# Optimization experiments

Hardware: AMD Instinct MI355X
Metric: run time of the kernel (lower is better)

Reference implementation:

```python
import jax, jax.numpy as jnp
import numpy as np

B, I, R, A, V = 256, 512, 512, 196, 10000

def _linear_params(key, out_dim, in_dim):
    k1, k2 = jax.random.split(key)
    s = 1.0 / np.sqrt(in_dim)
    W = jax.random.uniform(k1, (out_dim, in_dim), minval=-s, maxval=s, dtype=jnp.float32)
    b = jax.random.uniform(k2, (out_dim,), minval=-s, maxval=s, dtype=jnp.float32)
    return W, b

def setup_inputs() -> dict:
    key = jax.random.key(0)
    ks = jax.random.split(key, 16)
    d = {}
    d['x'] = jax.random.normal(ks[0], (B, I), dtype=jnp.float32)
    d['att'] = jax.random.normal(ks[1], (B, A, R), dtype=jnp.float32)
    d['prev_c'] = jax.random.normal(ks[2], (B, R), dtype=jnp.float32)
    d['prev_h'] = jax.random.normal(ks[3], (B, R), dtype=jnp.float32)
    for i, (name, o, inn) in enumerate([('a2a', A, R), ('h2a', A, R), ('d2d', 1, A),
                                         ('i2h', 4 * R, I), ('a2h', 4 * R, R), ('h2h', 4 * R, R),
                                         ('a2a1', A, R), ('h2a1', A, R), ('d2d1', 1, A),
                                         ('proj', V, R)]):
        W, b = _linear_params(ks[4 + i], o, inn)
        d['W_' + name] = W
        d['b_' + name] = b
    return d

def _lin(x, W, b):
    return x @ W.T + b

def _attend(att, h, Wa, ba, Wh, bh, Wd, bd):
    # att: (B, A, R); h: (B, R)
    av = jnp.einsum('bar,or->bao', att, Wa) + ba        # (B, A, A)
    ah = _lin(h, Wh, bh)                                # (B, A)
    dot = jnp.tanh(av + ah[:, :, None])                 # (B, A, A)
    scores = jnp.einsum('bao,o->ba', dot, Wd[0]) + bd[0]  # (B, A)
    w = jax.nn.softmax(scores, axis=-1)
    return jnp.einsum('bar,ba->br', att, w)             # (B, R)

def reference(x, att, prev_c, prev_h,
              W_a2a, b_a2a, W_h2a, b_h2a, W_d2d, b_d2d,
              W_i2h, b_i2h, W_a2h, b_a2h, W_h2h, b_h2h,
              W_a2a1, b_a2a1, W_h2a1, b_h2a1, W_d2d1, b_d2d1,
              W_proj, b_proj):
    # first attention uses prev_h
    prev_att_res = _attend(att, prev_h, W_a2a, b_a2a, W_h2a, b_h2a, W_d2d, b_d2d)
    sums = _lin(x, W_i2h, b_i2h) + _lin(prev_h, W_h2h, b_h2h) + _lin(prev_att_res, W_a2h, b_a2h)
    sig = jax.nn.sigmoid(sums[:, :3 * R])
    in_gate = sig[:, 0:R]
    forget_gate = sig[:, R:2 * R]
    out_gate = sig[:, 2 * R:3 * R]
    in_transform = jnp.tanh(sums[:, 3 * R:4 * R])
    next_c = forget_gate * prev_c + in_gate * in_transform
    next_h = out_gate * jnp.tanh(next_c)
    # second attention uses next_h
    att_res = _attend(att, next_h, W_a2a1, b_a2a1, W_h2a1, b_h2a1, W_d2d1, b_d2d1)
    top_h = att_res + next_h
    logsoft = jax.nn.log_softmax(_lin(top_h, W_proj, b_proj), axis=-1)
    return next_c, top_h, logsoft
```

## Files before the change

kernel.cpp:

```cpp
#include <hip/hip_runtime.h>
#include <math.h>

constexpr int cB  = 256;
constexpr int cI  = 512;
constexpr int cR  = 512;
constexpr int cA  = 196;
constexpr int cV  = 10000;
constexpr int cH4 = 2048;

typedef short bf16x8 __attribute__((ext_vector_type(8)));
typedef float f32x4  __attribute__((ext_vector_type(4)));
typedef unsigned short us8 __attribute__((ext_vector_type(8)));

__device__ inline unsigned short f2bf(float f) {
    unsigned int u = __float_as_uint(f);
    u += 0x7fffu + ((u >> 16) & 1u);
    return (unsigned short)(u >> 16);
}
__device__ inline float bf2f(unsigned short s) {
    return __uint_as_float(((unsigned int)s) << 16);
}

__global__ __launch_bounds__(256) void k_cvt4(
    const float* __restrict__ s0, unsigned short* __restrict__ d0, int nb0,
    const float* __restrict__ s1, unsigned short* __restrict__ d1, int nb1,
    const float* __restrict__ s2, unsigned short* __restrict__ d2, int nb2,
    const float* __restrict__ s3, unsigned short* __restrict__ d3, int nb3)
{
    int blk = blockIdx.x;
    const float* src; unsigned short* dst; int base;
    if (blk < nb0)                  { src = s0; dst = d0; base = blk; }
    else if (blk < nb0 + nb1)       { src = s1; dst = d1; base = blk - nb0; }
    else if (blk < nb0 + nb1 + nb2) { src = s2; dst = d2; base = blk - nb0 - nb1; }
    else                            { src = s3; dst = d3; base = blk - nb0 - nb1 - nb2; }
    int i = base * 256 + threadIdx.x;
    float4 v = ((const float4*)src)[i];
    ushort4 b;
    b.x = f2bf(v.x); b.y = f2bf(v.y); b.z = f2bf(v.z); b.w = f2bf(v.w);
    ((ushort4*)dst)[i] = b;
}

__global__ __launch_bounds__(256) void k_ah(
    const float* __restrict__ h, const float* __restrict__ W,
    const float* __restrict__ bias, float* __restrict__ out)
{
    __shared__ __align__(16) float h_s[cR];
    int b = blockIdx.x;
    int t = threadIdx.x;
    h_s[t]       = h[b * cR + t];
    h_s[t + 256] = h[b * cR + t + 256];
    __syncthreads();
    if (t < cA) {
        const float4* Wv = (const float4*)(W + (size_t)t * cR);
        const float4* hv = (const float4*)h_s;
        float acc = 0.f;
        #pragma unroll 4
        for (int k = 0; k < cR / 4; ++k) {
            float4 w4 = Wv[k], x4 = hv[k];
            acc += w4.x * x4.x + w4.y * x4.y + w4.z * x4.z + w4.w * x4.w;
        }
        out[b * cA + t] = acc + bias[t];
    }
}

constexpr int SC_LDA = 72;

__global__ __launch_bounds__(256, 3) void k_scores_cv(
    const float* __restrict__ att, unsigned short* __restrict__ att_bf,
    const unsigned short* __restrict__ wa_bf,
    const float* __restrict__ ba, const float* __restrict__ Wd,
    const float* __restrict__ bd, const float* __restrict__ ah,
    float* __restrict__ scores, int wb)
{
    __shared__ __align__(16) unsigned short att_s[64][SC_LDA];
    __shared__ __align__(16) unsigned short wa_s[224][SC_LDA];
    __shared__ float ba_s[224];
    __shared__ float wd_s[224];
    __shared__ float part_s[64][2];

    int tid  = threadIdx.x;
    int wave = tid >> 6;
    int lane = tid & 63;
    int lx   = lane & 15;
    int quad = lane >> 4;
    int mg   = wave >> 1;
    int ng   = wave & 1;
    size_t row0 = (size_t)blockIdx.x * 64;

    if (tid < 224) {
        ba_s[tid] = (tid < cA) ? ba[tid] : 0.f;
        wd_s[tid] = (tid < cA) ? Wd[tid] : 0.f;
    }

    int a_r = tid >> 4, a_c = (tid & 15) * 4;
    int w_r = tid >> 3, w_c = (tid & 7) * 8;
    const float* attA = att + (row0 + a_r) * cR + a_c;
    unsigned short* wbA = att_bf + (row0 + a_r) * cR + a_c;

    f32x4 acc[2][7];
    #pragma unroll
    for (int m = 0; m < 2; ++m)
        #pragma unroll
        for (int c = 0; c < 7; ++c) acc[m][c] = (f32x4){0.f, 0.f, 0.f, 0.f};

    float4 patt[4];
    us8    pwa[7];
    #pragma unroll
    for (int i = 0; i < 4; ++i)
        patt[i] = *(const float4*)(attA + (size_t)i * 16 * cR);
    #pragma unroll
    for (int i = 0; i < 7; ++i) {
        int r = w_r + 32 * i;
        pwa[i] = (r < cA) ? *(const us8*)(wa_bf + (size_t)r * cR + w_c)
                          : (us8){0,0,0,0,0,0,0,0};
    }

    for (int k0 = 0; k0 < cR; k0 += 64) {
        #pragma unroll
        for (int i = 0; i < 4; ++i) {
            float4 v = patt[i];
            ushort4 bv;
            bv.x = f2bf(v.x); bv.y = f2bf(v.y); bv.z = f2bf(v.z); bv.w = f2bf(v.w);
            *(ushort4*)&att_s[a_r + 16 * i][a_c] = bv;
            if (wb)
                *(ushort4*)(wbA + (size_t)i * 16 * cR + k0) = bv;
        }
        #pragma unroll
        for (int i = 0; i < 7; ++i)
            *(us8*)&wa_s[w_r + 32 * i][w_c] = pwa[i];
        if (k0 + 64 < cR) {
            #pragma unroll
            for (int i = 0; i < 4; ++i)
                patt[i] = *(const float4*)(attA + (size_t)i * 16 * cR + k0 + 64);
            #pragma unroll
            for (int i = 0; i < 7; ++i) {
                int r = w_r + 32 * i;
                pwa[i] = (r < cA) ? *(const us8*)(wa_bf + (size_t)r * cR + k0 + 64 + w_c)
                                  : (us8){0,0,0,0,0,0,0,0};
            }
        }
        __syncthreads();
        #pragma unroll
        for (int ks = 0; ks < 2; ++ks) {
            int kb = ks * 32 + quad * 8;
            bf16x8 af[2];
            #pragma unroll
            for (int m = 0; m < 2; ++m)
                af[m] = *(const bf16x8*)&att_s[mg * 32 + m * 16 + lx][kb];
            #pragma unroll
            for (int c = 0; c < 7; ++c) {
                bf16x8 bfr = *(const bf16x8*)&wa_s[ng * 112 + c * 16 + lx][kb];
                #pragma unroll
                for (int m = 0; m < 2; ++m)
                    acc[m][c] = __builtin_amdgcn_mfma_f32_16x16x32_bf16(af[m], bfr, acc[m][c], 0, 0, 0);
            }
        }
        __syncthreads();
    }

    #pragma unroll
    for (int m = 0; m < 2; ++m) {
        #pragma unroll
        for (int reg = 0; reg < 4; ++reg) {
            int rl = mg * 32 + m * 16 + quad * 4 + reg;
            float ahv = ah[row0 + rl];
            float part = 0.f;
            #pragma unroll
            for (int c = 0; c < 7; ++c) {
                int col = ng * 112 + c * 16 + lx;
                part += tanhf(acc[m][c][reg] + ba_s[col] + ahv) * wd_s[col];
            }
            part += __shfl_xor(part, 1);
            part += __shfl_xor(part, 2);
            part += __shfl_xor(part, 4);
            part += __shfl_xor(part, 8);
            if (lx == 0) part_s[rl][ng] = part;
        }
    }
    __syncthreads();
    if (tid < 64)
        scores[row0 + tid] = part_s[tid][0] + part_s[tid][1] + bd[0];
}

__global__ __launch_bounds__(256, 3) void k_scores_bf(
    const unsigned short* __restrict__ att_bf,
    const unsigned short* __restrict__ wa_bf,
    const float* __restrict__ ba, const float* __restrict__ Wd,
    const float* __restrict__ bd, const float* __restrict__ ah,
    float* __restrict__ scores)
{
    __shared__ __align__(16) unsigned short att_s[64][SC_LDA];
    __shared__ __align__(16) unsigned short wa_s[224][SC_LDA];
    __shared__ float ba_s[224];
    __shared__ float wd_s[224];
    __shared__ float part_s[64][2];

    int tid  = threadIdx.x;
    int wave = tid >> 6;
    int lane = tid & 63;
    int lx   = lane & 15;
    int quad = lane >> 4;
    int mg   = wave >> 1;
    int ng   = wave & 1;
    size_t row0 = (size_t)blockIdx.x * 64;

    if (tid < 224) {
        ba_s[tid] = (tid < cA) ? ba[tid] : 0.f;
        wd_s[tid] = (tid < cA) ? Wd[tid] : 0.f;
    }

    int a_r = tid >> 3, a_c = (tid & 7) * 8;
    int w_r = tid >> 3, w_c = (tid & 7) * 8;
    const unsigned short* attA = att_bf + (row0 + a_r) * cR + a_c;

    f32x4 acc[2][7];
    #pragma unroll
    for (int m = 0; m < 2; ++m)
        #pragma unroll
        for (int c = 0; c < 7; ++c) acc[m][c] = (f32x4){0.f, 0.f, 0.f, 0.f};

    us8 patt[2];
    us8 pwa[7];
    #pragma unroll
    for (int i = 0; i < 2; ++i)
        patt[i] = *(const us8*)(attA + (size_t)i * 32 * cR);
    #pragma unroll
    for (int i = 0; i < 7; ++i) {
        int r = w_r + 32 * i;
        pwa[i] = (r < cA) ? *(const us8*)(wa_bf + (size_t)r * cR + w_c)
                          : (us8){0,0,0,0,0,0,0,0};
    }

    for (int k0 = 0; k0 < cR; k0 += 64) {
        #pragma unroll
        for (int i = 0; i < 2; ++i)
            *(us8*)&att_s[a_r + 32 * i][a_c] = patt[i];
        #pragma unroll
        for (int i = 0; i < 7; ++i)
            *(us8*)&wa_s[w_r + 32 * i][w_c] = pwa[i];
        if (k0 + 64 < cR) {
            #pragma unroll
            for (int i = 0; i < 2; ++i)
                patt[i] = *(const us8*)(attA + (size_t)i * 32 * cR + k0 + 64);
            #pragma unroll
            for (int i = 0; i < 7; ++i) {
                int r = w_r + 32 * i;
                pwa[i] = (r < cA) ? *(const us8*)(wa_bf + (size_t)r * cR + k0 + 64 + w_c)
                                  : (us8){0,0,0,0,0,0,0,0};
            }
        }
        __syncthreads();
        #pragma unroll
        for (int ks = 0; ks < 2; ++ks) {
            int kb = ks * 32 + quad * 8;
            bf16x8 af[2];
            #pragma unroll
            for (int m = 0; m < 2; ++m)
                af[m] = *(const bf16x8*)&att_s[mg * 32 + m * 16 + lx][kb];
            #pragma unroll
            for (int c = 0; c < 7; ++c) {
                bf16x8 bfr = *(const bf16x8*)&wa_s[ng * 112 + c * 16 + lx][kb];
                #pragma unroll
                for (int m = 0; m < 2; ++m)
                    acc[m][c] = __builtin_amdgcn_mfma_f32_16x16x32_bf16(af[m], bfr, acc[m][c], 0, 0, 0);
            }
        }
        __syncthreads();
    }

    #pragma unroll
    for (int m = 0; m < 2; ++m) {
        #pragma unroll
        for (int reg = 0; reg < 4; ++reg) {
            int rl = mg * 32 + m * 16 + quad * 4 + reg;
            float ahv = ah[row0 + rl];
            float part = 0.f;
            #pragma unroll
            for (int c = 0; c < 7; ++c) {
                int col = ng * 112 + c * 16 + lx;
                part += tanhf(acc[m][c][reg] + ba_s[col] + ahv) * wd_s[col];
            }
            part += __shfl_xor(part, 1);
            part += __shfl_xor(part, 2);
            part += __shfl_xor(part, 4);
            part += __shfl_xor(part, 8);
            if (lx == 0) part_s[rl][ng] = part;
        }
    }
    __syncthreads();
    if (tid < 64)
        scores[row0 + tid] = part_s[tid][0] + part_s[tid][1] + bd[0];
}

__device__ inline void softmax_w(const float* scores, int b, int t, float* red,
                                 float* w_s)
{
    float s = (t < cA) ? scores[b * cA + t] : -INFINITY;
    red[t] = s; __syncthreads();
    for (int off = 128; off > 0; off >>= 1) {
        if (t < off) red[t] = fmaxf(red[t], red[t + off]);
        __syncthreads();
    }
    float mx = red[0];
    __syncthreads();
    float e = (t < cA) ? expf(s - mx) : 0.f;
    red[t] = e; __syncthreads();
    for (int off = 128; off > 0; off >>= 1) {
        if (t < off) red[t] += red[t + off];
        __syncthreads();
    }
    float inv = 1.f / red[0];
    if (t < cA) w_s[t] = e * inv;
    __syncthreads();
}

__global__ __launch_bounds__(512) void k_attres_bf(
    const float* __restrict__ scores, const unsigned short* __restrict__ att_bf,
    const float* __restrict__ addin,
    float* __restrict__ out, unsigned short* __restrict__ out_bf)
{
    __shared__ float red[512];
    __shared__ float w_s[cA];
    __shared__ float red2[8][512];
    int b = blockIdx.x, t = threadIdx.x;

    float s = (t < cA) ? scores[b * cA + t] : -INFINITY;
    red[t] = s; __syncthreads();
    for (int off = 256; off > 0; off >>= 1) {
        if (t < off) red[t] = fmaxf(red[t], red[t + off]);
        __syncthreads();
    }
    float mx = red[0];
    __syncthreads();
    float e = (t < cA) ? expf(s - mx) : 0.f;
    red[t] = e; __syncthreads();
    for (int off = 256; off > 0; off >>= 1) {
        if (t < off) red[t] += red[t + off];
        __syncthreads();
    }
    float inv = 1.f / red[0];
    if (t < cA) w_s[t] = e * inv;
    __syncthreads();

    int p = t >> 6, l = t & 63;
    const unsigned short* base = att_bf + (size_t)b * cA * cR + l * 8;
    float acc[8] = {};
    #pragma unroll 4
    for (int a = p; a < cA; a += 8) {
        us8 v = *(const us8*)(base + (size_t)a * cR);
        float w = w_s[a];
        #pragma unroll
        for (int j = 0; j < 8; ++j)
            acc[j] += bf2f(v[j]) * w;
    }
    #pragma unroll
    for (int j = 0; j < 8; ++j)
        red2[p][l * 8 + j] = acc[j];
    __syncthreads();
    {
        int r = t;
        float s2 = red2[0][r] + red2[1][r] + red2[2][r] + red2[3][r]
                 + red2[4][r] + red2[5][r] + red2[6][r] + red2[7][r];
        if (addin) s2 += addin[b * cR + r];
        out[b * cR + r] = s2;
        out_bf[b * cR + r] = f2bf(s2);
    }
}

__global__ __launch_bounds__(256) void k_attres_f32(
    const float* __restrict__ scores, const float* __restrict__ att,
    const float* __restrict__ addin,
    float* __restrict__ out, unsigned short* __restrict__ out_bf)
{
    __shared__ float red[256];
    __shared__ float w_s[cA];
    int b = blockIdx.x, t = threadIdx.x;
    softmax_w(scores, b, t, red, w_s);

    const float* attb = att + (size_t)b * cA * cR + 2 * t;
    float acc0 = 0.f, acc1 = 0.f;
    #pragma unroll 4
    for (int a = 0; a < cA; ++a) {
        float2 u = *(const float2*)(attb + (size_t)a * cR);
        float w = w_s[a];
        acc0 += u.x * w;
        acc1 += u.y * w;
    }
    if (addin) {
        acc0 += addin[b * cR + 2 * t];
        acc1 += addin[b * cR + 2 * t + 1];
    }
    out[b * cR + 2 * t]     = acc0;
    out[b * cR + 2 * t + 1] = acc1;
    out_bf[b * cR + 2 * t]     = f2bf(acc0);
    out_bf[b * cR + 2 * t + 1] = f2bf(acc1);
}

__global__ __launch_bounds__(256, 4) void k_sums(
    const unsigned short* __restrict__ x_bf,
    const unsigned short* __restrict__ h_bf,
    const unsigned short* __restrict__ ar_bf,
    const float* __restrict__ Wi, const float* __restrict__ Wh,
    const float* __restrict__ Wa,
    const float* __restrict__ bi, const float* __restrict__ bh,
    const float* __restrict__ ba, float* __restrict__ out)
{
    __shared__ __align__(16) unsigned short a_s[32][SC_LDA];
    __shared__ __align__(16) unsigned short w_s[64][SC_LDA];
    int tid  = threadIdx.x;
    int wave = tid >> 6;
    int lane = tid & 63;
    int lx   = lane & 15;
    int quad = lane >> 4;
    int b0 = blockIdx.x * 32;
    int j0 = blockIdx.y * 64;

    const unsigned short* Aarr[3] = {x_bf, h_bf, ar_bf};
    const float* Warr[3] = {Wi, Wh, Wa};

    int a_r = tid >> 3, a_c = (tid & 7) * 8;
    int w_r = tid >> 4, w_c = (tid & 15) * 4;

    f32x4 acc0 = {0.f, 0.f, 0.f, 0.f}, acc1 = {0.f, 0.f, 0.f, 0.f};

    us8 pa;
    float4 pw[4];
    pa = *(const us8*)(Aarr[0] + (size_t)(b0 + a_r) * cR + a_c);
    #pragma unroll
    for (int i = 0; i < 4; ++i)
        pw[i] = *(const float4*)(Warr[0] + (size_t)(j0 + w_r + 16 * i) * cR + w_c);

    for (int it = 0; it < 24; ++it) {
        *(us8*)&a_s[a_r][a_c] = pa;
        #pragma unroll
        for (int i = 0; i < 4; ++i) {
            float4 v = pw[i];
            ushort4 bv;
            bv.x = f2bf(v.x); bv.y = f2bf(v.y); bv.z = f2bf(v.z); bv.w = f2bf(v.w);
            *(ushort4*)&w_s[w_r + 16 * i][w_c] = bv;
        }
        if (it < 23) {
            int s2 = (it + 1) >> 3, k2 = ((it + 1) & 7) * 64;
            pa = *(const us8*)(Aarr[s2] + (size_t)(b0 + a_r) * cR + k2 + a_c);
            #pragma unroll
            for (int i = 0; i < 4; ++i)
                pw[i] = *(const float4*)(Warr[s2] + (size_t)(j0 + w_r + 16 * i) * cR + k2 + w_c);
        }
        __syncthreads();
        #pragma unroll
// ... 138 lines not shown
    float mx = -INFINITY;
    for (int v = t; v < cV / 4; v += 256) {
        float4 f = row4[v];
        mx = fmaxf(mx, fmaxf(fmaxf(f.x, f.y), fmaxf(f.z, f.w)));
    }
    red[t] = mx; __syncthreads();
    for (int off = 128; off > 0; off >>= 1) {
        if (t < off) red[t] = fmaxf(red[t], red[t + off]);
        __syncthreads();
    }
    mx = red[0]; __syncthreads();
    float sum = 0.f;
    for (int v = t; v < cV / 4; v += 256) {
        float4 f = row4[v];
        sum += expf(f.x - mx) + expf(f.y - mx) + expf(f.z - mx) + expf(f.w - mx);
    }
    red[t] = sum; __syncthreads();
    for (int off = 128; off > 0; off >>= 1) {
        if (t < off) red[t] += red[t + off];
        __syncthreads();
    }
    float lse = mx + logf(red[0]);
    for (int v = t; v < cV / 4; v += 256) {
        float4 f = row4[v];
        f.x -= lse; f.y -= lse; f.z -= lse; f.w -= lse;
        ((float4*)row)[v] = f;
    }
}

extern "C" void kernel_launch(void* const* d_in, const int* in_sizes, int n_in,
                              void* d_out, int out_size, void* d_ws, size_t ws_size,
                              hipStream_t stream)
{
    const float* x      = (const float*)d_in[0];
    const float* att    = (const float*)d_in[1];
    const float* prev_c = (const float*)d_in[2];
    const float* prev_h = (const float*)d_in[3];
    const float* W_a2a  = (const float*)d_in[4];
    const float* b_a2a  = (const float*)d_in[5];
    const float* W_h2a  = (const float*)d_in[6];
    const float* b_h2a  = (const float*)d_in[7];
    const float* W_d2d  = (const float*)d_in[8];
    const float* b_d2d  = (const float*)d_in[9];
    const float* W_i2h  = (const float*)d_in[10];
    const float* b_i2h  = (const float*)d_in[11];
    const float* W_a2h  = (const float*)d_in[12];
    const float* b_a2h  = (const float*)d_in[13];
    const float* W_h2h  = (const float*)d_in[14];
    const float* b_h2h  = (const float*)d_in[15];
    const float* W_a2a1 = (const float*)d_in[16];
    const float* b_a2a1 = (const float*)d_in[17];
    const float* W_h2a1 = (const float*)d_in[18];
    const float* b_h2a1 = (const float*)d_in[19];
    const float* W_d2d1 = (const float*)d_in[20];
    const float* b_d2d1 = (const float*)d_in[21];
    const float* W_proj = (const float*)d_in[22];
    const float* b_proj = (const float*)d_in[23];

    float* out_next_c = (float*)d_out;
    float* out_top_h  = out_next_c + (size_t)cB * cR;
    float* out_logits = out_top_h  + (size_t)cB * cR;

    const size_t ATT_FLOATS = 12845056;
    const size_t NEED_A = (ATT_FLOATS + 1445888) * sizeof(float);
    bool bigws = ws_size >= NEED_A;

    float* ws = (float*)d_ws;
    unsigned short* att_bf = (unsigned short*)ws;
    float* p = bigws ? (ws + ATT_FLOATS) : ws;
    unsigned short* wa2a_bf  = (unsigned short*)p;  p += 50176;
    unsigned short* wa2a1_bf = (unsigned short*)p;  p += 50176;
    unsigned short* x_bf     = (unsigned short*)p;  p += 65536;
    unsigned short* h_bf     = (unsigned short*)p;  p += 65536;
    unsigned short* ar1_bf   = (unsigned short*)p;  p += 65536;
    unsigned short* ar2_bf   = (unsigned short*)p;  p += 65536;
    unsigned short* toph_bf  = (unsigned short*)p;  p += 65536;
    float* ws_ah      = p;  p += 50176;
    float* ws_scores  = p;  p += 50176;
    float* ws_attres1 = p;  p += 131072;
    float* ws_attres2 = p;  p += 131072;
    float* ws_sums    = p;  p += 524288;
    float* ws_next_h  = p;  p += 131072;

    k_cvt4<<<452, 256, 0, stream>>>(W_a2a, wa2a_bf, 98,
                                    W_a2a1, wa2a1_bf, 98,
                                    x, x_bf, 128,
                                    prev_h, h_bf, 128);

    k_ah<<<cB, 256, 0, stream>>>(prev_h, W_h2a, b_h2a, ws_ah);
    k_scores_cv<<<(cB * cA) / 64, 256, 0, stream>>>(att, att_bf, wa2a_bf,
                                                    b_a2a, W_d2d, b_d2d,
                                                    ws_ah, ws_scores,
                                                    bigws ? 1 : 0);
    if (bigws)
        k_attres_bf<<<cB, 512, 0, stream>>>(ws_scores, att_bf, nullptr,
                                            ws_attres1, ar1_bf);
    else
        k_attres_f32<<<cB, 256, 0, stream>>>(ws_scores, att, nullptr,
                                             ws_attres1, ar1_bf);

    k_sums<<<dim3(8, 32), 256, 0, stream>>>(x_bf, h_bf, ar1_bf,
                                            W_i2h, W_h2h, W_a2h,
                                            b_i2h, b_h2h, b_a2h, ws_sums);
    k_cell<<<(cB * cR) / 256, 256, 0, stream>>>(ws_sums, prev_c, out_next_c, ws_next_h);

    k_ah<<<cB, 256, 0, stream>>>(ws_next_h, W_h2a1, b_h2a1, ws_ah);
    if (bigws) {
        k_scores_bf<<<(cB * cA) / 64, 256, 0, stream>>>(att_bf, wa2a1_bf,
                                                        b_a2a1, W_d2d1, b_d2d1,
                                                        ws_ah, ws_scores);
        k_attres_bf<<<cB, 512, 0, stream>>>(ws_scores, att_bf, ws_next_h,
                                            out_top_h, toph_bf);
    } else {
        k_scores_cv<<<(cB * cA) / 64, 256, 0, stream>>>(att, att_bf, wa2a1_bf,
                                                        b_a2a1, W_d2d1, b_d2d1,
                                                        ws_ah, ws_scores, 0);
        k_attres_f32<<<cB, 256, 0, stream>>>(ws_scores, att, ws_next_h,
                                             out_top_h, toph_bf);
    }

    k_lin<<<dim3(2, 157), 256, 0, stream>>>(toph_bf, W_proj, b_proj, out_logits, cV);
    k_logsoftmax<<<cB, 256, 0, stream>>>(out_logits);
}
```

Before: 389.0 us.

## Load whole att row tile into LDS up front in score kernels, halve M tile

The score kernels now process 32 att rows per block instead of 64 and load the full 512-wide row slice of att into shared memory once, before the K loop, instead of streaming 64-column chunks. Only the W_a2a tile is still pipelined per K step, and each wave now does one M fragment. The aim is to issue all att loads early for more memory-level parallelism and more blocks (twice the grid). In exchange the W_a2a tile is reloaded by twice as many blocks, register pressure rises from the 16 prefetched float4s, and occupancy is lowered to 2 blocks per CU.

```diff
diff --git a/kernel.cpp b/kernel.cpp
--- a/kernel.cpp
+++ b/kernel.cpp
@@ -64,19 +64,20 @@
 }
 
 constexpr int SC_LDA = 72;
-
-__global__ __launch_bounds__(256, 3) void k_scores_cv(
+constexpr int AT_LDA = 520;
+
+__global__ __launch_bounds__(256, 2) void k_scores_cv(
     const float* __restrict__ att, unsigned short* __restrict__ att_bf,
     const unsigned short* __restrict__ wa_bf,
     const float* __restrict__ ba, const float* __restrict__ Wd,
     const float* __restrict__ bd, const float* __restrict__ ah,
     float* __restrict__ scores, int wb)
 {
-    __shared__ __align__(16) unsigned short att_s[64][SC_LDA];
+    __shared__ __align__(16) unsigned short att_s[32][AT_LDA];
     __shared__ __align__(16) unsigned short wa_s[224][SC_LDA];
     __shared__ float ba_s[224];
     __shared__ float wd_s[224];
-    __shared__ float part_s[64][2];
+    __shared__ float part_s[32][2];
 
     int tid  = threadIdx.x;
     int wave = tid >> 6;
@@ -85,29 +86,18 @@
     int quad = lane >> 4;
     int mg   = wave >> 1;
     int ng   = wave & 1;
-    size_t row0 = (size_t)blockIdx.x * 64;
-
-    if (tid < 224) {
-        ba_s[tid] = (tid < cA) ? ba[tid] : 0.f;
-        wd_s[tid] = (tid < cA) ? Wd[tid] : 0.f;
-    }
-
-    int a_r = tid >> 4, a_c = (tid & 15) * 4;
+    size_t row0 = (size_t)blockIdx.x * 32;
+
+    const float* attW = att + (row0 + wave * 8) * cR + lane * 4;
+    float4 patt[16];
+    #pragma unroll
+    for (int i = 0; i < 8; ++i) {
+        patt[2 * i]     = *(const float4*)(attW + (size_t)i * cR);
+        patt[2 * i + 1] = *(const float4*)(attW + (size_t)i * cR + 256);
+    }
+
     int w_r = tid >> 3, w_c = (tid & 7) * 8;
-    const float* attA = att + (row0 + a_r) * cR + a_c;
-    unsigned short* wbA = att_bf + (row0 + a_r) * cR + a_c;
-
-    f32x4 acc[2][7];
-    #pragma unroll
-    for (int m = 0; m < 2; ++m)
-        #pragma unroll
-        for (int c = 0; c < 7; ++c) acc[m][c] = (f32x4){0.f, 0.f, 0.f, 0.f};
-
-    float4 patt[4];
-    us8    pwa[7];
-    #pragma unroll
-    for (int i = 0; i < 4; ++i)
-        patt[i] = *(const float4*)(attA + (size_t)i * 16 * cR);
+    us8 pwa[7];
     #pragma unroll
     for (int i = 0; i < 7; ++i) {
         int r = w_r + 32 * i;
@@ -115,23 +105,36 @@
                           : (us8){0,0,0,0,0,0,0,0};
     }
 
-    for (int k0 = 0; k0 < cR; k0 += 64) {
-        #pragma unroll
-        for (int i = 0; i < 4; ++i) {
-            float4 v = patt[i];
+    if (tid < 224) {
+        ba_s[tid] = (tid < cA) ? ba[tid] : 0.f;
+        wd_s[tid] = (tid < cA) ? Wd[tid] : 0.f;
+    }
+
+    unsigned short* wbW = att_bf + (row0 + wave * 8) * cR + lane * 4;
+    #pragma unroll
+    for (int i = 0; i < 8; ++i) {
+        #pragma unroll
+        for (int p = 0; p < 2; ++p) {
+            float4 v = patt[2 * i + p];
             ushort4 bv;
             bv.x = f2bf(v.x); bv.y = f2bf(v.y); bv.z = f2bf(v.z); bv.w = f2bf(v.w);
-            *(ushort4*)&att_s[a_r + 16 * i][a_c] = bv;
+            *(ushort4*)&att_s[wave * 8 + i][p * 256 + lane * 4] = bv;
             if (wb)
-                *(ushort4*)(wbA + (size_t)i * 16 * cR + k0) = bv;
-        }
+                *(ushort4*)(wbW + (size_t)i * cR + p * 256) = bv;
+        }
+    }
+
+    f32x4 acc[7];
+    #pragma unroll
+    for (int c = 0; c < 7; ++c) acc[c] = (f32x4){0.f, 0.f, 0.f, 0.f};
+
+    __syncthreads();
+
+    for (int k0 = 0; k0 < cR; k0 += 64) {
         #pragma unroll
         for (int i = 0; i < 7; ++i)
             *(us8*)&wa_s[w_r + 32 * i][w_c] = pwa[i];
         if (k0 + 64 < cR) {
-            #pragma unroll
-            for (int i = 0; i < 4; ++i)
-                patt[i] = *(const float4*)(attA + (size_t)i * 16 * cR + k0 + 64);
             #pragma unroll
             for (int i = 0; i < 7; ++i) {
                 int r = w_r + 32 * i;
@@ -143,57 +146,49 @@
         #pragma unroll
         for (int ks = 0; ks < 2; ++ks) {
             int kb = ks * 32 + quad * 8;
-            bf16x8 af[2];
-            #pragma unroll
-            for (int m = 0; m < 2; ++m)
-                af[m] = *(const bf16x8*)&att_s[mg * 32 + m * 16 + lx][kb];
+            bf16x8 af = *(const bf16x8*)&att_s[mg * 16 + lx][k0 + kb];
             #pragma unroll
             for (int c = 0; c < 7; ++c) {
                 bf16x8 bfr = *(const bf16x8*)&wa_s[ng * 112 + c * 16 + lx][kb];
-                #pragma unroll
-                for (int m = 0; m < 2; ++m)
-                    acc[m][c] = __builtin_amdgcn_mfma_f32_16x16x32_bf16(af[m], bfr, acc[m][c], 0, 0, 0);
+                acc[c] = __builtin_amdgcn_mfma_f32_16x16x32_bf16(af, bfr, acc[c], 0, 0, 0);
             }
         }
         __syncthreads();
     }
 
     #pragma unroll
-    for (int m = 0; m < 2; ++m) {
-        #pragma unroll
-        for (int reg = 0; reg < 4; ++reg) {
-            int rl = mg * 32 + m * 16 + quad * 4 + reg;
-            float ahv = ah[row0 + rl];
-            float part = 0.f;
-            #pragma unroll
-            for (int c = 0; c < 7; ++c) {
-                int col = ng * 112 + c * 16 + lx;
-                part += tanhf(acc[m][c][reg] + ba_s[col] + ahv) * wd_s[col];
-            }
-            part += __shfl_xor(part, 1);
-            part += __shfl_xor(part, 2);
-            part += __shfl_xor(part, 4);
-            part += __shfl_xor(part, 8);
-            if (lx == 0) part_s[rl][ng] = part;
-        }
-    }
-    __syncthreads();
-    if (tid < 64)
+    for (int reg = 0; reg < 4; ++reg) {
+        int rl = mg * 16 + quad * 4 + reg;
+        float ahv = ah[row0 + rl];
+        float part = 0.f;
+        #pragma unroll
+        for (int c = 0; c < 7; ++c) {
+            int col = ng * 112 + c * 16 + lx;
+            part += tanhf(acc[c][reg] + ba_s[col] + ahv) * wd_s[col];
+        }
+        part += __shfl_xor(part, 1);
+        part += __shfl_xor(part, 2);
+        part += __shfl_xor(part, 4);
+        part += __shfl_xor(part, 8);
+        if (lx == 0) part_s[rl][ng] = part;
+    }
+    __syncthreads();
+    if (tid < 32)
         scores[row0 + tid] = part_s[tid][0] + part_s[tid][1] + bd[0];
 }
 
-__global__ __launch_bounds__(256, 3) void k_scores_bf(
+__global__ __launch_bounds__(256, 2) void k_scores_bf(
     const unsigned short* __restrict__ att_bf,
     const unsigned short* __restrict__ wa_bf,
     const float* __restrict__ ba, const float* __restrict__ Wd,
     const float* __restrict__ bd, const float* __restrict__ ah,
     float* __restrict__ scores)
 {
-    __shared__ __align__(16) unsigned short att_s[64][SC_LDA];
+    __shared__ __align__(16) unsigned short att_s[32][AT_LDA];
     __shared__ __align__(16) unsigned short wa_s[224][SC_LDA];
     __shared__ float ba_s[224];
     __shared__ float wd_s[224];
-    __shared__ float part_s[64][2];
+    __shared__ float part_s[32][2];
 
     int tid  = threadIdx.x;
     int wave = tid >> 6;
@@ -202,28 +197,16 @@
     int quad = lane >> 4;
     int mg   = wave >> 1;
     int ng   = wave & 1;
-    size_t row0 = (size_t)blockIdx.x * 64;
-
-    if (tid < 224) {
-        ba_s[tid] = (tid < cA) ? ba[tid] : 0.f;
-        wd_s[tid] = (tid < cA) ? Wd[tid] : 0.f;
-    }
-
-    int a_r = tid >> 3, a_c = (tid & 7) * 8;
+    size_t row0 = (size_t)blockIdx.x * 32;
+
+    const unsigned short* attW = att_bf + (row0 + wave * 8) * cR + lane * 8;
+    us8 patt[8];
+    #pragma unroll
+    for (int i = 0; i < 8; ++i)
+        patt[i] = *(const us8*)(attW + (size_t)i * cR);
+
     int w_r = tid >> 3, w_c = (tid & 7) * 8;
-    const unsigned short* attA = att_bf + (row0 + a_r) * cR + a_c;
-
-    f32x4 acc[2][7];
-    #pragma unroll
-    for (int m = 0; m < 2; ++m)
-        #pragma unroll
-        for (int c = 0; c < 7; ++c) acc[m][c] = (f32x4){0.f, 0.f, 0.f, 0.f};
-
-    us8 patt[2];
     us8 pwa[7];
-    #pragma unroll
-    for (int i = 0; i < 2; ++i)
-        patt[i] = *(const us8*)(attA + (size_t)i * 32 * cR);
     #pragma unroll
     for (int i = 0; i < 7; ++i) {
         int r = w_r + 32 * i;
@@ -231,17 +214,26 @@
                           : (us8){0,0,0,0,0,0,0,0};
     }
 
+    if (tid < 224) {
+        ba_s[tid] = (tid < cA) ? ba[tid] : 0.f;
+        wd_s[tid] = (tid < cA) ? Wd[tid] : 0.f;
+    }
+
+    #pragma unroll
+    for (int i = 0; i < 8; ++i)
+        *(us8*)&att_s[wave * 8 + i][lane * 8] = patt[i];
+
+    f32x4 acc[7];
+    #pragma unroll
+    for (int c = 0; c < 7; ++c) acc[c] = (f32x4){0.f, 0.f, 0.f, 0.f};
+
+    __syncthreads();
+
     for (int k0 = 0; k0 < cR; k0 += 64) {
-        #pragma unroll
-        for (int i = 0; i < 2; ++i)
-            *(us8*)&att_s[a_r + 32 * i][a_c] = patt[i];
         #pragma unroll
         for (int i = 0; i < 7; ++i)
             *(us8*)&wa_s[w_r + 32 * i][w_c] = pwa[i];
         if (k0 + 64 < cR) {
-            #pragma unroll
-            for (int i = 0; i < 2; ++i)
-                patt[i] = *(const us8*)(attA + (size_t)i * 32 * cR + k0 + 64);
             #pragma unroll
             for (int i = 0; i < 7; ++i) {
                 int r = w_r + 32 * i;
@@ -253,42 +245,34 @@
         #pragma unroll
         for (int ks = 0; ks < 2; ++ks) {
             int kb = ks * 32 + quad * 8;
-            bf16x8 af[2];
-            #pragma unroll
-            for (int m = 0; m < 2; ++m)
-                af[m] = *(const bf16x8*)&att_s[mg * 32 + m * 16 + lx][kb];
+            bf16x8 af = *(const bf16x8*)&att_s[mg * 16 + lx][k0 + kb];
             #pragma unroll
             for (int c = 0; c < 7; ++c) {
                 bf16x8 bfr = *(const bf16x8*)&wa_s[ng * 112 + c * 16 + lx][kb];
-                #pragma unroll
-                for (int m = 0; m < 2; ++m)
-                    acc[m][c] = __builtin_amdgcn_mfma_f32_16x16x32_bf16(af[m], bfr, acc[m][c], 0, 0, 0);
+                acc[c] = __builtin_amdgcn_mfma_f32_16x16x32_bf16(af, bfr, acc[c], 0, 0, 0);
             }
         }
         __syncthreads();
     }
 
     #pragma unroll
-    for (int m = 0; m < 2; ++m) {
-        #pragma unroll
-        for (int reg = 0; reg < 4; ++reg) {
-            int rl = mg * 32 + m * 16 + quad * 4 + reg;
-            float ahv = ah[row0 + rl];
-            float part = 0.f;
-            #pragma unroll
-            for (int c = 0; c < 7; ++c) {
-                int col = ng * 112 + c * 16 + lx;
-                part += tanhf(acc[m][c][reg] + ba_s[col] + ahv) * wd_s[col];
-            }
-            part += __shfl_xor(part, 1);
-            part += __shfl_xor(part, 2);
-            part += __shfl_xor(part, 4);
-            part += __shfl_xor(part, 8);
-            if (lx == 0) part_s[rl][ng] = part;
-        }
-    }
-    __syncthreads();
-    if (tid < 64)
+    for (int reg = 0; reg < 4; ++reg) {
+        int rl = mg * 16 + quad * 4 + reg;
+        float ahv = ah[row0 + rl];
+        float part = 0.f;
+        #pragma unroll
+        for (int c = 0; c < 7; ++c) {
+            int col = ng * 112 + c * 16 + lx;
+            part += tanhf(acc[c][reg] + ba_s[col] + ahv) * wd_s[col];
+        }
+        part += __shfl_xor(part, 1);
+        part += __shfl_xor(part, 2);
+        part += __shfl_xor(part, 4);
+        part += __shfl_xor(part, 8);
+        if (lx == 0) part_s[rl][ng] = part;
+    }
+    __syncthreads();
+    if (tid < 32)
         scores[row0 + tid] = part_s[tid][0] + part_s[tid][1] + bd[0];
 }
 
@@ -675,7 +659,7 @@
                                     prev_h, h_bf, 128);
 
     k_ah<<<cB, 256, 0, stream>>>(prev_h, W_h2a, b_h2a, ws_ah);
-    k_scores_cv<<<(cB * cA) / 64, 256, 0, stream>>>(att, att_bf, wa2a_bf,
+    k_scores_cv<<<(cB * cA) / 32, 256, 0, stream>>>(att, att_bf, wa2a_bf,
                                                     b_a2a, W_d2d, b_d2d,
                                                     ws_ah, ws_scores,
                                                     bigws ? 1 : 0);
@@ -693,13 +677,13 @@
 
     k_ah<<<cB, 256, 0, stream>>>(ws_next_h, W_h2a1, b_h2a1, ws_ah);
     if (bigws) {
-        k_scores_bf<<<(cB * cA) / 64, 256, 0, stream>>>(att_bf, wa2a1_bf,
+        k_scores_bf<<<(cB * cA) / 32, 256, 0, stream>>>(att_bf, wa2a1_bf,
                                                         b_a2a1, W_d2d1, b_d2d1,
                                                         ws_ah, ws_scores);
         k_attres_bf<<<cB, 512, 0, stream>>>(ws_scores, att_bf, ws_next_h,
                                             out_top_h, toph_bf);
     } else {
-        k_scores_cv<<<(cB * cA) / 64, 256, 0, stream>>>(att, att_bf, wa2a1_bf,
+        k_scores_cv<<<(cB * cA) / 32, 256, 0, stream>>>(att, att_bf, wa2a1_bf,
                                                         b_a2a1, W_d2d1, b_d2d1,
                                                         ws_ah, ws_scores, 0);
         k_attres_f32<<<cB, 256, 0, stream>>>(ws_scores, att, ws_next_h,
```

New measurement: 404.5 us. 4.0% more time.

## Fuse attention scores, softmax and weighted sum into split-softmax kernels

Applied to the files above, without the earlier changes.

Replaces the separate scores and attention-result kernels with fused kernels. Each block keeps 49 attention rows of one batch in shared memory as bf16, computes scores with MFMA against a streamed W_a2a, does a partial softmax and a weighted sum, then writes partial numerators and max/denominator values. A small finalize kernel merges the four partials per batch using flash-style rescaling. This avoids rereading att from global memory for the weighted sum and removes the scores round trip. It also swaps tanhf for an exp-based tanh. In exchange, 64-row tiles hold only 49 valid rows, and the large shared footprint allows one block per CU.

```diff
diff --git a/kernel.cpp b/kernel.cpp
--- a/kernel.cpp
+++ b/kernel.cpp
@@ -19,6 +19,9 @@
 }
 __device__ inline float bf2f(unsigned short s) {
     return __uint_as_float(((unsigned int)s) << 16);
+}
+__device__ inline float tanh_f(float x) {
+    return 1.f - 2.f / (1.f + __expf(2.f * x));
 }
 
 __global__ __launch_bounds__(256) void k_cvt4(
@@ -64,6 +67,322 @@
 }
 
 constexpr int SC_LDA = 72;
+constexpr int AT_LDA = 520;
+
+
+__global__ __launch_bounds__(256, 1) void k_attf1(
+    const float* __restrict__ att, unsigned short* __restrict__ att_bf,
+    const unsigned short* __restrict__ wa_bf,
+    const float* __restrict__ ba, const float* __restrict__ Wd,
+    const float* __restrict__ bd, const float* __restrict__ ah,
+    float* __restrict__ pnum, float* __restrict__ pm, float* __restrict__ pden)
+{
+    __shared__ __align__(16) unsigned short att_s[64][AT_LDA];
+    __shared__ __align__(16) unsigned short wa_s[32][AT_LDA];
+    __shared__ float ba_s[224];
+    __shared__ float wd_s[224];
+    __shared__ float s_sc[64];
+    __shared__ float s_e[64];
+    __shared__ float red2[4][512];
+
+    int tid  = threadIdx.x;
+    int wave = tid >> 6;
+    int lane = tid & 63;
+    int lx   = lane & 15;
+    int quad = lane >> 4;
+    int blk  = blockIdx.x;
+    int b    = blk >> 2;
+    int a0   = (blk & 3) * 49;
+    size_t rowbase = (size_t)b * cA + a0;
+    const float* abase = att + rowbase * cR;
+    unsigned short* wbase = att_bf + rowbase * cR;
+    float bd0 = bd[0];
+
+    if (tid < 224) {
+        ba_s[tid] = (tid < cA) ? ba[tid] : 0.f;
+        wd_s[tid] = (tid < cA) ? Wd[tid] : 0.f;
+    }
+
+    float ahv[4];
+    int arow = wave * 16 + quad * 4;
+    #pragma unroll
+    for (int reg = 0; reg < 4; ++reg) {
+        int al = arow + reg;
+        ahv[reg] = (al < 49) ? ah[b * cA + a0 + al] : 0.f;
+    }
+
+    us8 pwa[8];
+    #pragma unroll
+    for (int i = 0; i < 8; ++i) {
+        int u = tid + i * 256;
+        pwa[i] = *(const us8*)(wa_bf + (size_t)(u >> 6) * cR + (u & 63) * 8);
+    }
+
+    #pragma unroll 8
+    for (int i = 0; i < 24; ++i) {
+        int u = tid + i * 256;
+        float4 v = *(const float4*)(abase + (size_t)u * 4);
+        ushort4 bv;
+        bv.x = f2bf(v.x); bv.y = f2bf(v.y); bv.z = f2bf(v.z); bv.w = f2bf(v.w);
+        *(ushort4*)&att_s[u >> 7][(u & 127) * 4] = bv;
+        *(ushort4*)(wbase + (size_t)u * 4) = bv;
+    }
+    {
+        int u = tid + 24 * 256;
+        if (u < 49 * 128) {
+            float4 v = *(const float4*)(abase + (size_t)u * 4);
+            ushort4 bv;
+            bv.x = f2bf(v.x); bv.y = f2bf(v.y); bv.z = f2bf(v.z); bv.w = f2bf(v.w);
+            *(ushort4*)&att_s[u >> 7][(u & 127) * 4] = bv;
+            *(ushort4*)(wbase + (size_t)u * 4) = bv;
+        }
+    }
+
+    float part[4] = {0.f, 0.f, 0.f, 0.f};
+
+    for (int ch = 0; ch < 7; ++ch) {
+        #pragma unroll
+        for (int i = 0; i < 8; ++i) {
+            int u = tid + i * 256;
+            *(us8*)&wa_s[u >> 6][(u & 63) * 8] = pwa[i];
+        }
+        if (ch < 6) {
+            int c0n = (ch + 1) * 32;
+            #pragma unroll
+            for (int i = 0; i < 8; ++i) {
+                int u = tid + i * 256;
+                int r = c0n + (u >> 6);
+                pwa[i] = (r < cA) ? *(const us8*)(wa_bf + (size_t)r * cR + (u & 63) * 8)
+                                  : (us8){0,0,0,0,0,0,0,0};
+            }
+        }
+        __syncthreads();
+
+        f32x4 acc0 = {0.f,0.f,0.f,0.f}, acc1 = {0.f,0.f,0.f,0.f};
+        #pragma unroll
+        for (int ks = 0; ks < 16; ++ks) {
+            int kb = ks * 32 + quad * 8;
+            bf16x8 af = *(const bf16x8*)&att_s[wave * 16 + lx][kb];
+            bf16x8 b0 = *(const bf16x8*)&wa_s[lx][kb];
+            bf16x8 b1 = *(const bf16x8*)&wa_s[16 + lx][kb];
+            acc0 = __builtin_amdgcn_mfma_f32_16x16x32_bf16(af, b0, acc0, 0, 0, 0);
+            acc1 = __builtin_amdgcn_mfma_f32_16x16x32_bf16(af, b1, acc1, 0, 0, 0);
+        }
+        int c0 = ch * 32;
+        #pragma unroll
+        for (int reg = 0; reg < 4; ++reg) {
+            part[reg] += tanh_f(acc0[reg] + ba_s[c0 + lx] + ahv[reg]) * wd_s[c0 + lx];
+            part[reg] += tanh_f(acc1[reg] + ba_s[c0 + 16 + lx] + ahv[reg]) * wd_s[c0 + 16 + lx];
+        }
+        __syncthreads();
+    }
+
+    #pragma unroll
+    for (int reg = 0; reg < 4; ++reg) {
+        float p = part[reg];
+        p += __shfl_xor(p, 1);
+        p += __shfl_xor(p, 2);
+        p += __shfl_xor(p, 4);
+        p += __shfl_xor(p, 8);
+        if (lx == 0) s_sc[wave * 16 + quad * 4 + reg] = p + bd0;
+    }
+    __syncthreads();
+
+    float m = s_sc[0];
+    #pragma unroll 8
+    for (int a = 1; a < 49; ++a) m = fmaxf(m, s_sc[a]);
+    if (tid < 49) s_e[tid] = __expf(s_sc[tid] - m);
+    __syncthreads();
+    float den = 0.f;
+    #pragma unroll 8
+    for (int a = 0; a < 49; ++a) den += s_e[a];
+
+    float num8[8] = {};
+    for (int a = wave; a < 49; a += 4) {
+        float e = s_e[a];
+        us8 v = *(const us8*)&att_s[a][lane * 8];
+        #pragma unroll
+        for (int j = 0; j < 8; ++j)
+            num8[j] += e * bf2f(v[j]);
+    }
+    #pragma unroll
+    for (int j = 0; j < 8; ++j)
+        red2[wave][lane * 8 + j] = num8[j];
+    __syncthreads();
+    #pragma unroll
+    for (int rr = 0; rr < 2; ++rr) {
+        int c = tid + rr * 256;
+        pnum[(size_t)blk * cR + c] = red2[0][c] + red2[1][c] + red2[2][c] + red2[3][c];
+    }
+    if (tid == 0) { pm[blk] = m; pden[blk] = den; }
+}
+
+__global__ __launch_bounds__(256, 1) void k_attf2(
+    const unsigned short* __restrict__ att_bf,
+    const unsigned short* __restrict__ wa_bf,
+    const float* __restrict__ ba, const float* __restrict__ Wd,
+    const float* __restrict__ bd, const float* __restrict__ ah,
+    float* __restrict__ pnum, float* __restrict__ pm, float* __restrict__ pden)
+{
+    __shared__ __align__(16) unsigned short att_s[64][AT_LDA];
+    __shared__ __align__(16) unsigned short wa_s[32][AT_LDA];
+    __shared__ float ba_s[224];
+    __shared__ float wd_s[224];
+    __shared__ float s_sc[64];
+    __shared__ float s_e[64];
+    __shared__ float red2[4][512];
+
+    int tid  = threadIdx.x;
+    int wave = tid >> 6;
+    int lane = tid & 63;
+    int lx   = lane & 15;
+    int quad = lane >> 4;
+    int blk  = blockIdx.x;
+    int b    = blk >> 2;
+    int a0   = (blk & 3) * 49;
+    size_t rowbase = (size_t)b * cA + a0;
+    const unsigned short* abase = att_bf + rowbase * cR;
+    float bd0 = bd[0];
+
+    if (tid < 224) {
+        ba_s[tid] = (tid < cA) ? ba[tid] : 0.f;
+        wd_s[tid] = (tid < cA) ? Wd[tid] : 0.f;
+    }
+
+    float ahv[4];
+    int arow = wave * 16 + quad * 4;
+    #pragma unroll
+    for (int reg = 0; reg < 4; ++reg) {
+        int al = arow + reg;
+        ahv[reg] = (al < 49) ? ah[b * cA + a0 + al] : 0.f;
+    }
+
+    us8 pwa[8];
+    #pragma unroll
+    for (int i = 0; i < 8; ++i) {
+        int u = tid + i * 256;
+        pwa[i] = *(const us8*)(wa_bf + (size_t)(u >> 6) * cR + (u & 63) * 8);
+    }
+
+    #pragma unroll 6
+    for (int i = 0; i < 12; ++i) {
+        int u = tid + i * 256;
+        us8 v = *(const us8*)(abase + (size_t)u * 8);
+        *(us8*)&att_s[u >> 6][(u & 63) * 8] = v;
+    }
+    {
+        int u = tid + 12 * 256;
+        if (u < 49 * 64) {
+            us8 v = *(const us8*)(abase + (size_t)u * 8);
+            *(us8*)&att_s[u >> 6][(u & 63) * 8] = v;
+        }
+    }
+
+    float part[4] = {0.f, 0.f, 0.f, 0.f};
+
+    for (int ch = 0; ch < 7; ++ch) {
+        #pragma unroll
+        for (int i = 0; i < 8; ++i) {
+            int u = tid + i * 256;
+            *(us8*)&wa_s[u >> 6][(u & 63) * 8] = pwa[i];
+        }
+        if (ch < 6) {
+            int c0n = (ch + 1) * 32;
+            #pragma unroll
+            for (int i = 0; i < 8; ++i) {
+                int u = tid + i * 256;
+                int r = c0n + (u >> 6);
+                pwa[i] = (r < cA) ? *(const us8*)(wa_bf + (size_t)r * cR + (u & 63) * 8)
+                                  : (us8){0,0,0,0,0,0,0,0};
+            }
+        }
+        __syncthreads();
+
+        f32x4 acc0 = {0.f,0.f,0.f,0.f}, acc1 = {0.f,0.f,0.f,0.f};
+        #pragma unroll
+        for (int ks = 0; ks < 16; ++ks) {
+            int kb = ks * 32 + quad * 8;
+            bf16x8 af = *(const bf16x8*)&att_s[wave * 16 + lx][kb];
+            bf16x8 b0 = *(const bf16x8*)&wa_s[lx][kb];
+            bf16x8 b1 = *(const bf16x8*)&wa_s[16 + lx][kb];
+            acc0 = __builtin_amdgcn_mfma_f32_16x16x32_bf16(af, b0, acc0, 0, 0, 0);
+            acc1 = __builtin_amdgcn_mfma_f32_16x16x32_bf16(af, b1, acc1, 0, 0, 0);
+        }
+        int c0 = ch * 32;
+        #pragma unroll
+        for (int reg = 0; reg < 4; ++reg) {
+            part[reg] += tanh_f(acc0[reg] + ba_s[c0 + lx] + ahv[reg]) * wd_s[c0 + lx];
+            part[reg] += tanh_f(acc1[reg] + ba_s[c0 + 16 + lx] + ahv[reg]) * wd_s[c0 + 16 + lx];
+        }
+        __syncthreads();
+    }
+
+    #pragma unroll
+    for (int reg = 0; reg < 4; ++reg) {
+        float p = part[reg];
+        p += __shfl_xor(p, 1);
+        p += __shfl_xor(p, 2);
+        p += __shfl_xor(p, 4);
+        p += __shfl_xor(p, 8);
+        if (lx == 0) s_sc[wave * 16 + quad * 4 + reg] = p + bd0;
+    }
+    __syncthreads();
+
+    float m = s_sc[0];
+    #pragma unroll 8
+    for (int a = 1; a < 49; ++a) m = fmaxf(m, s_sc[a]);
+    if (tid < 49) s_e[tid] = __expf(s_sc[tid] - m);
+    __syncthreads();
+    float den = 0.f;
+    #pragma unroll 8
+    for (int a = 0; a < 49; ++a) den += s_e[a];
+
+    float num8[8] = {};
+    for (int a = wave; a < 49; a += 4) {
+        float e = s_e[a];
+        us8 v = *(const us8*)&att_s[a][lane * 8];
+        #pragma unroll
+        for (int j = 0; j < 8; ++j)
+            num8[j] += e * bf2f(v[j]);
+    }
+    #pragma unroll
+    for (int j = 0; j < 8; ++j)
+        red2[wave][lane * 8 + j] = num8[j];
+    __syncthreads();
+    #pragma unroll
+    for (int rr = 0; rr < 2; ++rr) {
+        int c = tid + rr * 256;
+        pnum[(size_t)blk * cR + c] = red2[0][c] + red2[1][c] + red2[2][c] + red2[3][c];
+    }
+    if (tid == 0) { pm[blk] = m; pden[blk] = den; }
+}
+
+__global__ __launch_bounds__(256) void k_attfin(
+    const float* __restrict__ pnum, const float* __restrict__ pm,
+    const float* __restrict__ pden, const float* __restrict__ addin,
+    float* __restrict__ out, unsigned short* __restrict__ out_bf)
+{
+    int b = blockIdx.x, t = threadIdx.x;
+    int base = b * 4;
+    float m0 = pm[base], m1 = pm[base+1], m2 = pm[base+2], m3 = pm[base+3];
+    float M = fmaxf(fmaxf(m0, m1), fmaxf(m2, m3));
+    float w0 = __expf(m0 - M), w1 = __expf(m1 - M);
+    float w2 = __expf(m2 - M), w3 = __expf(m3 - M);
+    float D = w0 * pden[base] + w1 * pden[base+1] + w2 * pden[base+2] + w3 * pden[base+3];
+    float inv = 1.f / D;
+    #pragma unroll
+    for (int rr = 0; rr < 2; ++rr) {
+        int c = t + rr * 256;
+        float s = w0 * pnum[(size_t)(base+0) * cR + c]
+                + w1 * pnum[(size_t)(base+1) * cR + c]
+                + w2 * pnum[(size_t)(base+2) * cR + c]
+                + w3 * pnum[(size_t)(base+3) * cR + c];
+        s *= inv;
+        if (addin) s += addin[b * cR + c];
+        out[b * cR + c] = s;
+        out_bf[b * cR + c] = f2bf(s);
+    }
+}
 
 __global__ __launch_bounds__(256, 3) void k_scores_cv(
     const float* __restrict__ att, unsigned short* __restrict__ att_bf,
@@ -182,116 +501,6 @@
         scores[row0 + tid] = part_s[tid][0] + part_s[tid][1] + bd[0];
 }
 
-__global__ __launch_bounds__(256, 3) void k_scores_bf(
-    const unsigned short* __restrict__ att_bf,
-    const unsigned short* __restrict__ wa_bf,
-    const float* __restrict__ ba, const float* __restrict__ Wd,
-    const float* __restrict__ bd, const float* __restrict__ ah,
-    float* __restrict__ scores)
-{
-    __shared__ __align__(16) unsigned short att_s[64][SC_LDA];
-    __shared__ __align__(16) unsigned short wa_s[224][SC_LDA];
-    __shared__ float ba_s[224];
-    __shared__ float wd_s[224];
-    __shared__ float part_s[64][2];
-
-    int tid  = threadIdx.x;
-    int wave = tid >> 6;
-    int lane = tid & 63;
-    int lx   = lane & 15;
-    int quad = lane >> 4;
-    int mg   = wave >> 1;
-    int ng   = wave & 1;
-    size_t row0 = (size_t)blockIdx.x * 64;
-
-    if (tid < 224) {
-        ba_s[tid] = (tid < cA) ? ba[tid] : 0.f;
-        wd_s[tid] = (tid < cA) ? Wd[tid] : 0.f;
-    }
-
-    int a_r = tid >> 3, a_c = (tid & 7) * 8;
-    int w_r = tid >> 3, w_c = (tid & 7) * 8;
-    const unsigned short* attA = att_bf + (row0 + a_r) * cR + a_c;
-
-    f32x4 acc[2][7];
-    #pragma unroll
-    for (int m = 0; m < 2; ++m)
-        #pragma unroll
-        for (int c = 0; c < 7; ++c) acc[m][c] = (f32x4){0.f, 0.f, 0.f, 0.f};
-
-    us8 patt[2];
-    us8 pwa[7];
-    #pragma unroll
-    for (int i = 0; i < 2; ++i)
-        patt[i] = *(const us8*)(attA + (size_t)i * 32 * cR);
-    #pragma unroll
-    for (int i = 0; i < 7; ++i) {
-        int r = w_r + 32 * i;
-        pwa[i] = (r < cA) ? *(const us8*)(wa_bf + (size_t)r * cR + w_c)
-                          : (us8){0,0,0,0,0,0,0,0};
-    }
-
-    for (int k0 = 0; k0 < cR; k0 += 64) {
-        #pragma unroll
-        for (int i = 0; i < 2; ++i)
-            *(us8*)&att_s[a_r + 32 * i][a_c] = patt[i];
-        #pragma unroll
-        for (int i = 0; i < 7; ++i)
-            *(us8*)&wa_s[w_r + 32 * i][w_c] = pwa[i];
-        if (k0 + 64 < cR) {
-            #pragma unroll
-            for (int i = 0; i < 2; ++i)
-                patt[i] = *(const us8*)(attA + (size_t)i * 32 * cR + k0 + 64);
-            #pragma unroll
-            for (int i = 0; i < 7; ++i) {
-                int r = w_r + 32 * i;
-                pwa[i] = (r < cA) ? *(const us8*)(wa_bf + (size_t)r * cR + k0 + 64 + w_c)
-                                  : (us8){0,0,0,0,0,0,0,0};
-            }
-        }
-        __syncthreads();
-        #pragma unroll
-        for (int ks = 0; ks < 2; ++ks) {
-            int kb = ks * 32 + quad * 8;
-            bf16x8 af[2];
-            #pragma unroll
-            for (int m = 0; m < 2; ++m)
-                af[m] = *(const bf16x8*)&att_s[mg * 32 + m * 16 + lx][kb];
-            #pragma unroll
-            for (int c = 0; c < 7; ++c) {
-                bf16x8 bfr = *(const bf16x8*)&wa_s[ng * 112 + c * 16 + lx][kb];
-                #pragma unroll
-                for (int m = 0; m < 2; ++m)
-                    acc[m][c] = __builtin_amdgcn_mfma_f32_16x16x32_bf16(af[m], bfr, acc[m][c], 0, 0, 0);
-            }
-        }
-        __syncthreads();
-    }
-
-    #pragma unroll
-    for (int m = 0; m < 2; ++m) {
-        #pragma unroll
-        for (int reg = 0; reg < 4; ++reg) {
-            int rl = mg * 32 + m * 16 + quad * 4 + reg;
-            float ahv = ah[row0 + rl];
-            float part = 0.f;
-            #pragma unroll
-            for (int c = 0; c < 7; ++c) {
-                int col = ng * 112 + c * 16 + lx;
-                part += tanhf(acc[m][c][reg] + ba_s[col] + ahv) * wd_s[col];
-            }
-            part += __shfl_xor(part, 1);
-            part += __shfl_xor(part, 2);
-            part += __shfl_xor(part, 4);
-            part += __shfl_xor(part, 8);
-            if (lx == 0) part_s[rl][ng] = part;
-        }
-    }
-    __syncthreads();
-    if (tid < 64)
-        scores[row0 + tid] = part_s[tid][0] + part_s[tid][1] + bd[0];
-}
-
 __device__ inline void softmax_w(const float* scores, int b, int t, float* red,
                                  float* w_s)
 {
@@ -312,59 +521,6 @@
     float inv = 1.f / red[0];
     if (t < cA) w_s[t] = e * inv;
     __syncthreads();
-}
-
-__global__ __launch_bounds__(512) void k_attres_bf(
-    const float* __restrict__ scores, const unsigned short* __restrict__ att_bf,
-    const float* __restrict__ addin,
-    float* __restrict__ out, unsigned short* __restrict__ out_bf)
-{
-    __shared__ float red[512];
-    __shared__ float w_s[cA];
-    __shared__ float red2[8][512];
-    int b = blockIdx.x, t = threadIdx.x;
-
-    float s = (t < cA) ? scores[b * cA + t] : -INFINITY;
-    red[t] = s; __syncthreads();
-    for (int off = 256; off > 0; off >>= 1) {
-        if (t < off) red[t] = fmaxf(red[t], red[t + off]);
-        __syncthreads();
-    }
-    float mx = red[0];
-    __syncthreads();
-    float e = (t < cA) ? expf(s - mx) : 0.f;
-    red[t] = e; __syncthreads();
-    for (int off = 256; off > 0; off >>= 1) {
-        if (t < off) red[t] += red[t + off];
-        __syncthreads();
-    }
-    float inv = 1.f / red[0];
-    if (t < cA) w_s[t] = e * inv;
-    __syncthreads();
-
-    int p = t >> 6, l = t & 63;
-    const unsigned short* base = att_bf + (size_t)b * cA * cR + l * 8;
-    float acc[8] = {};
-    #pragma unroll 4
-    for (int a = p; a < cA; a += 8) {
-        us8 v = *(const us8*)(base + (size_t)a * cR);
-        float w = w_s[a];
-        #pragma unroll
-        for (int j = 0; j < 8; ++j)
-            acc[j] += bf2f(v[j]) * w;
-    }
-    #pragma unroll
-    for (int j = 0; j < 8; ++j)
-        red2[p][l * 8 + j] = acc[j];
-    __syncthreads();
-    {
-        int r = t;
-        float s2 = red2[0][r] + red2[1][r] + red2[2][r] + red2[3][r]
-                 + red2[4][r] + red2[5][r] + red2[6][r] + red2[7][r];
-        if (addin) s2 += addin[b * cR + r];
-        out[b * cR + r] = s2;
-        out_bf[b * cR + r] = f2bf(s2);
-    }
 }
 
 __global__ __launch_bounds__(256) void k_attres_f32(
@@ -669,22 +825,29 @@
     float* ws_sums    = p;  p += 524288;
     float* ws_next_h  = p;  p += 131072;
 
+    float* pnum = ws_sums;
+    float* pm   = ws_scores;
+    float* pden = ws_scores + 1024;
+
     k_cvt4<<<452, 256, 0, stream>>>(W_a2a, wa2a_bf, 98,
                                     W_a2a1, wa2a1_bf, 98,
                                     x, x_bf, 128,
                                     prev_h, h_bf, 128);
 
     k_ah<<<cB, 256, 0, stream>>>(prev_h, W_h2a, b_h2a, ws_ah);
-    k_scores_cv<<<(cB * cA) / 64, 256, 0, stream>>>(att, att_bf, wa2a_bf,
-                                                    b_a2a, W_d2d, b_d2d,
-                                                    ws_ah, ws_scores,
-                                                    bigws ? 1 : 0);
-    if (bigws)
-        k_attres_bf<<<cB, 512, 0, stream>>>(ws_scores, att_bf, nullptr,
-                                            ws_attres1, ar1_bf);
-    else
+    if (bigws) {
+        k_attf1<<<cB * 4, 256, 0, stream>>>(att, att_bf, wa2a_bf,
+                                            b_a2a, W_d2d, b_d2d, ws_ah,
+                                            pnum, pm, pden);
+        k_attfin<<<cB, 256, 0, stream>>>(pnum, pm, pden, nullptr,
+                                         ws_attres1, ar1_bf);
+    } else {
+        k_scores_cv<<<(cB * cA) / 64, 256, 0, stream>>>(att, att_bf, wa2a_bf,
+                                                        b_a2a, W_d2d, b_d2d,
+                                                        ws_ah, ws_scores, 0);
         k_attres_f32<<<cB, 256, 0, stream>>>(ws_scores, att, nullptr,
                                              ws_attres1, ar1_bf);
+    }
 
     k_sums<<<dim3(8, 32), 256, 0, stream>>>(x_bf, h_bf, ar1_bf,
                                             W_i2h, W_h2h, W_a2h,
@@ -693,11 +856,11 @@
 
     k_ah<<<cB, 256, 0, stream>>>(ws_next_h, W_h2a1, b_h2a1, ws_ah);
     if (bigws) {
-        k_scores_bf<<<(cB * cA) / 64, 256, 0, stream>>>(att_bf, wa2a1_bf,
-                                                        b_a2a1, W_d2d1, b_d2d1,
-                                                        ws_ah, ws_scores);
-        k_attres_bf<<<cB, 512, 0, stream>>>(ws_scores, att_bf, ws_next_h,
-                                            out_top_h, toph_bf);
+        k_attf2<<<cB * 4, 256, 0, stream>>>(att_bf, wa2a1_bf,
+                                            b_a2a1, W_d2d1, b_d2d1, ws_ah,
+                                            pnum, pm, pden);
+        k_attfin<<<cB, 256, 0, stream>>>(pnum, pm, pden, ws_next_h,
+                                         out_top_h, toph_bf);
     } else {
         k_scores_cv<<<(cB * cA) / 64, 256, 0, stream>>>(att, att_bf, wa2a1_bf,
                                                         b_a2a1, W_d2d1, b_d2d1,
```

New measurement: 505.0 us. 29.8% more time.
